# Kernel tuning notes

Hardware: AMD Instinct MI355X
Metric: run time of the kernel (lower is better)

The kernel has to match this reference:

```python
import jax, jax.numpy as jnp
import numpy as np

RANK = 16
ALPHA = 32
SCALING = ALPHA / RANK  # 2.0


def setup_inputs() -> dict:
    key = jax.random.key(0)
    k1, k2, k3 = jax.random.split(key, 3)
    B_, S, D, O = 2, 4096, 4096, 4096
    x = jax.random.normal(k1, (B_, S, D), dtype=jnp.float32)
    # Dequantized base weight, torch Linear layout [out, in]
    W_base = jax.random.normal(k2, (O, D), dtype=jnp.float32) * 0.02
    # kaiming_uniform-ish init for lora_A [rank, in]
    bound = float(np.sqrt(6.0 / (1 + 5) / D))
    A = jax.random.uniform(k3, (RANK, D), dtype=jnp.float32, minval=-bound, maxval=bound)
    # lora_B initialized to zeros [out, rank]
    Bm = jnp.zeros((O, RANK), dtype=jnp.float32)
    return {"x": x, "W_base": W_base, "A": A, "B": Bm}


def reference(x, W_base, A, B):
    # Y = x @ W_base^T + (x @ A^T) @ B^T * scaling   (dropout p=0 -> identity)
    base_out = jnp.einsum('bsd,od->bso', x, W_base)
    lora_mid = jnp.einsum('bsd,rd->bsr', x, A)        # [B,S,rank]
    lora_out = jnp.einsum('bsr,or->bso', lora_mid, B) # [B,S,out]
    return base_out + lora_out * SCALING
```

## Files before the change

### kernel.cpp

```cpp
#include <hip/hip_runtime.h>
#include <hip/hip_bf16.h>

typedef __attribute__((ext_vector_type(8))) __bf16 bf16x8;
typedef __attribute__((ext_vector_type(4))) float  f32x4;

__global__ __launch_bounds__(256) void cvt_f32_bf16(
    const float* __restrict__ in, __bf16* __restrict__ out, long n8)
{
    long i = (long)blockIdx.x * blockDim.x + threadIdx.x;
    long stride = (long)gridDim.x * blockDim.x;
    for (; i < n8; i += stride) {
        const f32x4* p = (const f32x4*)(in + i * 8);
        f32x4 a = p[0], b = p[1];
        bf16x8 o;
        o[0] = (__bf16)a[0]; o[1] = (__bf16)a[1];
        o[2] = (__bf16)a[2]; o[3] = (__bf16)a[3];
        o[4] = (__bf16)b[0]; o[5] = (__bf16)b[1];
        o[6] = (__bf16)b[2]; o[7] = (__bf16)b[3];
        *(bf16x8*)(out + i * 8) = o;
    }
}

__global__ __launch_bounds__(256) void mid_and_cvt(
    const float* __restrict__ x, const float* __restrict__ A,
    float* __restrict__ mid, __bf16* __restrict__ Xb, int K, int M)
{
    int tid = threadIdx.x;
    int m0 = blockIdx.x * 4;

    float acc[4][16];
#pragma unroll
    for (int row = 0; row < 4; ++row)
#pragma unroll
        for (int r = 0; r < 16; ++r) acc[row][r] = 0.f;

    int iters = K / 2048;
    for (int it = 0; it < iters; ++it) {
        int k = it * 2048 + tid * 8;
        f32x4 xv[4][2];
#pragma unroll
        for (int row = 0; row < 4; ++row) {
            if (m0 + row < M) {
                const float* xr = x + (size_t)(m0 + row) * K;
                xv[row][0] = *(const f32x4*)(xr + k);
                xv[row][1] = *(const f32x4*)(xr + k + 4);
            } else {
                f32x4 z = {0.f,0.f,0.f,0.f};
                xv[row][0] = z; xv[row][1] = z;
            }
            if (Xb && m0 + row < M) {
                bf16x8 o;
                o[0] = (__bf16)xv[row][0][0]; o[1] = (__bf16)xv[row][0][1];
                o[2] = (__bf16)xv[row][0][2]; o[3] = (__bf16)xv[row][0][3];
                o[4] = (__bf16)xv[row][1][0]; o[5] = (__bf16)xv[row][1][1];
                o[6] = (__bf16)xv[row][1][2]; o[7] = (__bf16)xv[row][1][3];
                *(bf16x8*)(Xb + (size_t)(m0 + row) * K + k) = o;
            }
        }
#pragma unroll
        for (int r = 0; r < 16; ++r) {
            const f32x4* ap = (const f32x4*)(A + (size_t)r * K + k);
            f32x4 a0 = ap[0], a1 = ap[1];
#pragma unroll
            for (int row = 0; row < 4; ++row) {
                acc[row][r] += xv[row][0][0]*a0[0] + xv[row][0][1]*a0[1]
                             + xv[row][0][2]*a0[2] + xv[row][0][3]*a0[3]
                             + xv[row][1][0]*a1[0] + xv[row][1][1]*a1[1]
                             + xv[row][1][2]*a1[2] + xv[row][1][3]*a1[3];
            }
        }
    }

#pragma unroll
    for (int row = 0; row < 4; ++row)
#pragma unroll
        for (int r = 0; r < 16; ++r)
#pragma unroll
            for (int off = 32; off > 0; off >>= 1)
                acc[row][r] += __shfl_down(acc[row][r], off, 64);

    __shared__ float red[4][4][16];
    int lane = tid & 63, w = tid >> 6;
    if (lane == 0) {
#pragma unroll
        for (int row = 0; row < 4; ++row)
#pragma unroll
            for (int r = 0; r < 16; ++r) red[w][row][r] = acc[row][r];
    }
    __syncthreads();
    if (tid < 64) {
        int row = tid >> 4, r = tid & 15;
        if (m0 + row < M) {
            float s = red[0][row][r] + red[1][row][r]
                    + red[2][row][r] + red[3][row][r];
            mid[(size_t)(m0 + row) * 16 + r] = s;
        }
    }
}

#define GL16(g, l) __builtin_amdgcn_global_load_lds( \
    (const __attribute__((address_space(1))) void*)(g), \
    (__attribute__((address_space(3))) void*)(l), 16, 0, 0)

__global__ __launch_bounds__(512, 2) void gemm256(
    const __bf16* __restrict__ Xb,
    const __bf16* __restrict__ Wb,
    const float*  __restrict__ mid,
    const float*  __restrict__ Bl,
    float* __restrict__ out,
    int M, int N, int K)
{
    __shared__ __bf16 As[4][256 * 32];
    __shared__ __bf16 Bs[4][256 * 32];

    const int NT = K >> 5;

    int nbx = N >> 8, nby = M >> 8, nwg = nbx * nby;
    int bid = blockIdx.x, swz = bid;
    if ((nwg & 7) == 0) { int cpx = nwg >> 3; swz = (bid & 7) * cpx + (bid >> 3); }
    int by = swz / nbx, bx = swz % nbx;
    int m0 = by << 8, n0 = bx << 8;

    int tid = threadIdx.x;
    int lane = tid & 63;
    int w = tid >> 6;
    int wm = w >> 2, wn = w & 3;

    int q0 = tid >> 2;
    int c0 = tid & 3;
    int csrc = c0 ^ ((q0 >> 1) & 3);
    const __bf16* sA0 = Xb + (size_t)(m0 + q0) * K + csrc * 8;
    const __bf16* sA1 = sA0 + (size_t)128 * K;
    const __bf16* sB0 = Wb + (size_t)(n0 + q0) * K + csrc * 8;
    const __bf16* sB1 = sB0 + (size_t)128 * K;
    unsigned ldsw = (unsigned)w * 1024;

    int chunkSwz = (lane >> 4) ^ ((lane >> 1) & 3);
    unsigned aoff = (unsigned)((wm * 128 + (lane & 15)) * 64 + chunkSwz * 16);
    unsigned boff = (unsigned)((wn * 64  + (lane & 15)) * 64 + chunkSwz * 16);

    f32x4 acc[8][4];
    {
        int kh = lane >> 4;
        bf16x8 bI[4];
#pragma unroll
        for (int j = 0; j < 4; ++j) {
            bf16x8 v = {};
            if (kh < 2) {
                int col = n0 + wn * 64 + j * 16 + (lane & 15);
                const f32x4* p = (const f32x4*)(Bl + (size_t)col * 16 + kh * 8);
                f32x4 v0 = p[0], v1 = p[1];
                v[0] = (__bf16)(2.0f * v0[0]); v[1] = (__bf16)(2.0f * v0[1]);
                v[2] = (__bf16)(2.0f * v0[2]); v[3] = (__bf16)(2.0f * v0[3]);
                v[4] = (__bf16)(2.0f * v1[0]); v[5] = (__bf16)(2.0f * v1[1]);
                v[6] = (__bf16)(2.0f * v1[2]); v[7] = (__bf16)(2.0f * v1[3]);
            }
            bI[j] = v;
        }
#pragma unroll
        for (int i = 0; i < 8; ++i) {
            bf16x8 aI = {};
            if (kh < 2) {
                int row = m0 + wm * 128 + i * 16 + (lane & 15);
                const f32x4* p = (const f32x4*)(mid + (size_t)row * 16 + kh * 8);
                f32x4 v0 = p[0], v1 = p[1];
                aI[0] = (__bf16)v0[0]; aI[1] = (__bf16)v0[1];
                aI[2] = (__bf16)v0[2]; aI[3] = (__bf16)v0[3];
                aI[4] = (__bf16)v1[0]; aI[5] = (__bf16)v1[1];
                aI[6] = (__bf16)v1[2]; aI[7] = (__bf16)v1[3];
            }
            f32x4 z = {0.f, 0.f, 0.f, 0.f};
#pragma unroll
            for (int j = 0; j < 4; ++j)
                acc[i][j] = __builtin_amdgcn_mfma_f32_16x16x32_bf16(aI, bI[j], z, 0, 0, 0);
        }
    }

    GL16(sA0, (char*)As[0] + ldsw);
    GL16(sA1, (char*)As[0] + 8192 + ldsw);
    GL16(sB0, (char*)Bs[0] + ldsw);
    GL16(sB1, (char*)Bs[0] + 8192 + ldsw);
    GL16(sA0 + 32, (char*)As[1] + ldsw);
    GL16(sA1 + 32, (char*)As[1] + 8192 + ldsw);
    GL16(sB0 + 32, (char*)Bs[1] + ldsw);
    GL16(sB1 + 32, (char*)Bs[1] + 8192 + ldsw);
    asm volatile("s_waitcnt vmcnt(4)" ::: "memory");
    asm volatile("s_barrier" ::: "memory");

    int cur = 0;
    for (int t = 0; t < NT; ++t) {
        const __bf16* bufA = As[cur];
        const __bf16* bufB = Bs[cur];
        bool pf = (t + 2) < NT;
        int pb = (t + 2) & 3;
        size_t koff = (size_t)(t + 2) * 32;

        if (pf) {
            GL16(sA0 + koff, (char*)As[pb] + ldsw);
            GL16(sA1 + koff, (char*)As[pb] + 8192 + ldsw);
            GL16(sB0 + koff, (char*)Bs[pb] + ldsw);
            GL16(sB1 + koff, (char*)Bs[pb] + 8192 + ldsw);
        }

        bf16x8 bfr[4], af[8];
#pragma unroll
        for (int j = 0; j < 4; ++j)
            bfr[j] = *(const bf16x8*)((const char*)bufB + boff + j * 1024u);
#pragma unroll
        for (int i = 0; i < 8; ++i)
            af[i] = *(const bf16x8*)((const char*)bufA + aoff + i * 1024u);

        __builtin_amdgcn_s_setprio(1);
#pragma unroll
        for (int i = 0; i < 8; ++i)
#pragma unroll
            for (int j = 0; j < 4; ++j)
                acc[i][j] = __builtin_amdgcn_mfma_f32_16x16x32_bf16(
                    af[i], bfr[j], acc[i][j], 0, 0, 0);
        __builtin_amdgcn_s_setprio(0);

        if (pf) asm volatile("s_waitcnt vmcnt(4)" ::: "memory");
        else    asm volatile("s_waitcnt vmcnt(0)" ::: "memory");
        asm volatile("s_barrier" ::: "memory");

        cur = (cur + 1) & 3;
    }

#pragma unroll
    for (int i = 0; i < 8; ++i) {
        int rbase = m0 + wm * 128 + i * 16 + ((lane >> 4) << 2);
#pragma unroll
        for (int q = 0; q < 4; ++q) {
            float* orow = out + (size_t)(rbase + q) * N;
            int colb = n0 + wn * 64 + (lane & 15);
            orow[colb]      = acc[i][0][q];
            orow[colb + 16] = acc[i][1][q];
            orow[colb + 32] = acc[i][2][q];
            orow[colb + 48] = acc[i][3][q];
        }
    }
}

__global__ __launch_bounds__(256) void gemm_fb(
    const float* __restrict__ X, const float* __restrict__ W,
    const float* __restrict__ mid, const float* __restrict__ Bl,
    float* __restrict__ out, int M, int N, int K)
{
    __shared__ float As[64][16];
    __shared__ float Bs[64][16];
    int nbx = N / 64;
    int bx = blockIdx.x % nbx, by = blockIdx.x / nbx;
    int m0 = by * 64, n0 = bx * 64;
    int tid = threadIdx.x;
    int tr = tid >> 4, tc = tid & 15;

    float acc[4][4] = {};
    for (int kt = 0; kt < K; kt += 16) {
#pragma unroll
        for (int s = 0; s < 4; ++s) {
            int c = s * 256 + tid;
            int row = c >> 4, kk = c & 15;
            As[row][kk] = X[(size_t)(m0 + row) * K + kt + kk];
            Bs[row][kk] = W[(size_t)(n0 + row) * K + kt + kk];
        }
        __syncthreads();
#pragma unroll
        for (int kk = 0; kk < 16; ++kk) {
            float av[4], bv[4];
#pragma unroll
            for (int i = 0; i < 4; ++i) { av[i] = As[tr*4+i][kk]; bv[i] = Bs[tc*4+i][kk]; }
#pragma unroll
            for (int i = 0; i < 4; ++i)
#pragma unroll
                for (int j = 0; j < 4; ++j) acc[i][j] += av[i] * bv[j];
        }
        __syncthreads();
    }
#pragma unroll
    for (int i = 0; i < 4; ++i) {
        int row = m0 + tr * 4 + i;
#pragma unroll
        for (int j = 0; j < 4; ++j) {
            int col = n0 + tc * 4 + j;
            float s = 0.f;
#pragma unroll
            for (int r = 0; r < 16; ++r)
                s += mid[(size_t)row * 16 + r] * Bl[(size_t)col * 16 + r];
            out[(size_t)row * N + col] = acc[i][j] + 2.0f * s;
        }
    }
}

extern "C" void kernel_launch(void* const* d_in, const int* in_sizes, int n_in,
                              void* d_out, int out_size, void* d_ws, size_t ws_size,
                              hipStream_t stream)
{
    const float* x   = (const float*)d_in[0];
    const float* Wf  = (const float*)d_in[1];
    const float* A   = (const float*)d_in[2];
    const float* Bl  = (const float*)d_in[3];
    float* out = (float*)d_out;

    int D = in_sizes[2] / 16;
    int O = in_sizes[3] / 16;
    long M = (long)in_sizes[0] / D;
    int K = D, N = O;

    size_t xb_bytes  = (size_t)M * K * 2;
    size_t wb_bytes  = (size_t)N * K * 2;
    size_t mid_bytes = (size_t)M * 16 * 4;

    bool shapes_ok = (M % 256 == 0) && (N % 256 == 0) && (K % 2048 == 0);

    int midgrid = (int)((M + 3) / 4);

    if (shapes_ok && ws_size >= xb_bytes + wb_bytes + mid_bytes) {
        __bf16* Xb  = (__bf16*)d_ws;
        __bf16* Wbb = (__bf16*)((char*)d_ws + xb_bytes);
        float*  mid = (float*)((char*)d_ws + xb_bytes + wb_bytes);

        cvt_f32_bf16<<<2048, 256, 0, stream>>>(Wf, Wbb, (long)N * K / 8);
        mid_and_cvt<<<midgrid, 256, 0, stream>>>(x, A, mid, Xb, K, (int)M);
        int nwg = (int)(M / 256) * (N / 256);
        gemm256<<<nwg, 512, 0, stream>>>(Xb, Wbb, mid, Bl, out, (int)M, N, K);
    } else {
        float* mid = (float*)d_ws;
        mid_and_cvt<<<midgrid, 256, 0, stream>>>(x, A, mid, nullptr, K, (int)M);
        int nwg = (int)(M / 64) * (N / 64);
        gemm_fb<<<nwg, 256, 0, stream>>>(x, Wf, mid, Bl, out, (int)M, N, K);
    }
}
```

Measured before the change: 405.9 us.

## Software-pipeline LDS fragment loads with MFMA in half-tile phases, unroll by two

Restructures the main K loop of the 256x256 GEMM into an unrolled-by-two, four-phase schedule. LDS fragment reads for the next half-tile and the split A/B global_load_lds prefetches are interleaved between groups of 16 MFMAs. The goal is to hide LDS read latency behind matrix work, in the style of ping-pong scheduling. The cost is more barriers per iteration, higher register pressure from double fragment sets, and a dependence on NT being even plus careful vmcnt accounting.

```diff
diff --git a/kernel.cpp b/kernel.cpp
--- a/kernel.cpp
+++ b/kernel.cpp
@@ -102,6 +102,8 @@
     (const __attribute__((address_space(1))) void*)(g), \
     (__attribute__((address_space(3))) void*)(l), 16, 0, 0)
 
+#define LD8(base, off) (*(const bf16x8*)((const char*)(base) + (off)))
+
 __global__ __launch_bounds__(512, 2) void gemm256(
     const __bf16* __restrict__ Xb,
     const __bf16* __restrict__ Wb,
@@ -138,6 +140,13 @@
     int chunkSwz = (lane >> 4) ^ ((lane >> 1) & 3);
     unsigned aoff = (unsigned)((wm * 128 + (lane & 15)) * 64 + chunkSwz * 16);
     unsigned boff = (unsigned)((wn * 64  + (lane & 15)) * 64 + chunkSwz * 16);
+
+#define STAGE_A(t, b) do { size_t ko = (size_t)(t) * 32; \
+    GL16(sA0 + ko, (char*)As[b] + ldsw); \
+    GL16(sA1 + ko, (char*)As[b] + 8192 + ldsw); } while (0)
+#define STAGE_B(t, b) do { size_t ko = (size_t)(t) * 32; \
+    GL16(sB0 + ko, (char*)Bs[b] + ldsw); \
+    GL16(sB1 + ko, (char*)Bs[b] + 8192 + ldsw); } while (0)
 
     f32x4 acc[8][4];
     {
@@ -176,54 +185,142 @@
         }
     }
 
-    GL16(sA0, (char*)As[0] + ldsw);
-    GL16(sA1, (char*)As[0] + 8192 + ldsw);
-    GL16(sB0, (char*)Bs[0] + ldsw);
-    GL16(sB1, (char*)Bs[0] + 8192 + ldsw);
-    GL16(sA0 + 32, (char*)As[1] + ldsw);
-    GL16(sA1 + 32, (char*)As[1] + 8192 + ldsw);
-    GL16(sB0 + 32, (char*)Bs[1] + ldsw);
-    GL16(sB1 + 32, (char*)Bs[1] + 8192 + ldsw);
+    STAGE_A(0, 0); STAGE_B(0, 0);
+    STAGE_A(1, 1); STAGE_B(1, 1);
     asm volatile("s_waitcnt vmcnt(4)" ::: "memory");
     asm volatile("s_barrier" ::: "memory");
 
-    int cur = 0;
-    for (int t = 0; t < NT; ++t) {
-        const __bf16* bufA = As[cur];
-        const __bf16* bufB = Bs[cur];
-        bool pf = (t + 2) < NT;
-        int pb = (t + 2) & 3;
-        size_t koff = (size_t)(t + 2) * 32;
-
-        if (pf) {
-            GL16(sA0 + koff, (char*)As[pb] + ldsw);
-            GL16(sA1 + koff, (char*)As[pb] + 8192 + ldsw);
-            GL16(sB0 + koff, (char*)Bs[pb] + ldsw);
-            GL16(sB1 + koff, (char*)Bs[pb] + 8192 + ldsw);
-        }
-
-        bf16x8 bfr[4], af[8];
-#pragma unroll
-        for (int j = 0; j < 4; ++j)
-            bfr[j] = *(const bf16x8*)((const char*)bufB + boff + j * 1024u);
-#pragma unroll
-        for (int i = 0; i < 8; ++i)
-            af[i] = *(const bf16x8*)((const char*)bufA + aoff + i * 1024u);
-
+    bf16x8 axf0 = LD8(As[0], aoff);
+    bf16x8 axf1 = LD8(As[0], aoff + 1024);
+    bf16x8 axf2 = LD8(As[0], aoff + 2048);
+    bf16x8 axf3 = LD8(As[0], aoff + 3072);
+    bf16x8 bxf0 = LD8(Bs[0], boff);
+    bf16x8 bxf1 = LD8(Bs[0], boff + 1024);
+    bf16x8 bxf2 = LD8(Bs[0], boff + 2048);
+    bf16x8 bxf3 = LD8(Bs[0], boff + 3072);
+
+    for (int t = 0; t < NT; t += 2) {
+        const char* cA0 = (const char*)As[t & 3];
+        const char* cA1 = (const char*)As[(t + 1) & 3];
+        const char* cB1 = (const char*)Bs[(t + 1) & 3];
+        const char* cA2 = (const char*)As[(t + 2) & 3];
+        const char* cB2 = (const char*)Bs[(t + 2) & 3];
+        bool p2 = (t + 2) < NT;
+        bool p3 = (t + 3) < NT;
+
+        bf16x8 ax4 = LD8(cA0, aoff + 4096);
+        bf16x8 ax5 = LD8(cA0, aoff + 5120);
+        bf16x8 ax6 = LD8(cA0, aoff + 6144);
+        bf16x8 ax7 = LD8(cA0, aoff + 7168);
+        if (p2) STAGE_A(t + 2, (t + 2) & 3);
+        asm volatile("s_barrier" ::: "memory");
         __builtin_amdgcn_s_setprio(1);
-#pragma unroll
-        for (int i = 0; i < 8; ++i)
-#pragma unroll
-            for (int j = 0; j < 4; ++j)
-                acc[i][j] = __builtin_amdgcn_mfma_f32_16x16x32_bf16(
-                    af[i], bfr[j], acc[i][j], 0, 0, 0);
+        acc[0][0] = __builtin_amdgcn_mfma_f32_16x16x32_bf16(axf0, bxf0, acc[0][0], 0, 0, 0);
+        acc[0][1] = __builtin_amdgcn_mfma_f32_16x16x32_bf16(axf0, bxf1, acc[0][1], 0, 0, 0);
+        acc[0][2] = __builtin_amdgcn_mfma_f32_16x16x32_bf16(axf0, bxf2, acc[0][2], 0, 0, 0);
+        acc[0][3] = __builtin_amdgcn_mfma_f32_16x16x32_bf16(axf0, bxf3, acc[0][3], 0, 0, 0);
+        acc[1][0] = __builtin_amdgcn_mfma_f32_16x16x32_bf16(axf1, bxf0, acc[1][0], 0, 0, 0);
+        acc[1][1] = __builtin_amdgcn_mfma_f32_16x16x32_bf16(axf1, bxf1, acc[1][1], 0, 0, 0);
+        acc[1][2] = __builtin_amdgcn_mfma_f32_16x16x32_bf16(axf1, bxf2, acc[1][2], 0, 0, 0);
+        acc[1][3] = __builtin_amdgcn_mfma_f32_16x16x32_bf16(axf1, bxf3, acc[1][3], 0, 0, 0);
+        acc[2][0] = __builtin_amdgcn_mfma_f32_16x16x32_bf16(axf2, bxf0, acc[2][0], 0, 0, 0);
+        acc[2][1] = __builtin_amdgcn_mfma_f32_16x16x32_bf16(axf2, bxf1, acc[2][1], 0, 0, 0);
+        acc[2][2] = __builtin_amdgcn_mfma_f32_16x16x32_bf16(axf2, bxf2, acc[2][2], 0, 0, 0);
+        acc[2][3] = __builtin_amdgcn_mfma_f32_16x16x32_bf16(axf2, bxf3, acc[2][3], 0, 0, 0);
+        acc[3][0] = __builtin_amdgcn_mfma_f32_16x16x32_bf16(axf3, bxf0, acc[3][0], 0, 0, 0);
+        acc[3][1] = __builtin_amdgcn_mfma_f32_16x16x32_bf16(axf3, bxf1, acc[3][1], 0, 0, 0);
+        acc[3][2] = __builtin_amdgcn_mfma_f32_16x16x32_bf16(axf3, bxf2, acc[3][2], 0, 0, 0);
+        acc[3][3] = __builtin_amdgcn_mfma_f32_16x16x32_bf16(axf3, bxf3, acc[3][3], 0, 0, 0);
         __builtin_amdgcn_s_setprio(0);
 
-        if (pf) asm volatile("s_waitcnt vmcnt(4)" ::: "memory");
+        if (p2) STAGE_B(t + 2, (t + 2) & 3);
+        if (p2) asm volatile("s_waitcnt vmcnt(4)" ::: "memory");
         else    asm volatile("s_waitcnt vmcnt(0)" ::: "memory");
+        bf16x8 ayf0 = LD8(cA1, aoff);
+        bf16x8 ayf1 = LD8(cA1, aoff + 1024);
+        bf16x8 ayf2 = LD8(cA1, aoff + 2048);
+        bf16x8 ayf3 = LD8(cA1, aoff + 3072);
+        bf16x8 byf0 = LD8(cB1, boff);
+        bf16x8 byf1 = LD8(cB1, boff + 1024);
+        bf16x8 byf2 = LD8(cB1, boff + 2048);
+        bf16x8 byf3 = LD8(cB1, boff + 3072);
         asm volatile("s_barrier" ::: "memory");
-
-        cur = (cur + 1) & 3;
+        __builtin_amdgcn_s_setprio(1);
+        acc[4][0] = __builtin_amdgcn_mfma_f32_16x16x32_bf16(ax4, bxf0, acc[4][0], 0, 0, 0);
+        acc[4][1] = __builtin_amdgcn_mfma_f32_16x16x32_bf16(ax4, bxf1, acc[4][1], 0, 0, 0);
+        acc[4][2] = __builtin_amdgcn_mfma_f32_16x16x32_bf16(ax4, bxf2, acc[4][2], 0, 0, 0);
+        acc[4][3] = __builtin_amdgcn_mfma_f32_16x16x32_bf16(ax4, bxf3, acc[4][3], 0, 0, 0);
+        acc[5][0] = __builtin_amdgcn_mfma_f32_16x16x32_bf16(ax5, bxf0, acc[5][0], 0, 0, 0);
+        acc[5][1] = __builtin_amdgcn_mfma_f32_16x16x32_bf16(ax5, bxf1, acc[5][1], 0, 0, 0);
+        acc[5][2] = __builtin_amdgcn_mfma_f32_16x16x32_bf16(ax5, bxf2, acc[5][2], 0, 0, 0);
+        acc[5][3] = __builtin_amdgcn_mfma_f32_16x16x32_bf16(ax5, bxf3, acc[5][3], 0, 0, 0);
+        acc[6][0] = __builtin_amdgcn_mfma_f32_16x16x32_bf16(ax6, bxf0, acc[6][0], 0, 0, 0);
+        acc[6][1] = __builtin_amdgcn_mfma_f32_16x16x32_bf16(ax6, bxf1, acc[6][1], 0, 0, 0);
+        acc[6][2] = __builtin_amdgcn_mfma_f32_16x16x32_bf16(ax6, bxf2, acc[6][2], 0, 0, 0);
+        acc[6][3] = __builtin_amdgcn_mfma_f32_16x16x32_bf16(ax6, bxf3, acc[6][3], 0, 0, 0);
+        acc[7][0] = __builtin_amdgcn_mfma_f32_16x16x32_bf16(ax7, bxf0, acc[7][0], 0, 0, 0);
+        acc[7][1] = __builtin_amdgcn_mfma_f32_16x16x32_bf16(ax7, bxf1, acc[7][1], 0, 0, 0);
+        acc[7][2] = __builtin_amdgcn_mfma_f32_16x16x32_bf16(ax7, bxf2, acc[7][2], 0, 0, 0);
+        acc[7][3] = __builtin_amdgcn_mfma_f32_16x16x32_bf16(ax7, bxf3, acc[7][3], 0, 0, 0);
+        __builtin_amdgcn_s_setprio(0);
+
+        bf16x8 ay4 = LD8(cA1, aoff + 4096);
+        bf16x8 ay5 = LD8(cA1, aoff + 5120);
+        bf16x8 ay6 = LD8(cA1, aoff + 6144);
+        bf16x8 ay7 = LD8(cA1, aoff + 7168);
+        if (p3) STAGE_A(t + 3, (t + 3) & 3);
+        asm volatile("s_barrier" ::: "memory");
+        __builtin_amdgcn_s_setprio(1);
+        acc[0][0] = __builtin_amdgcn_mfma_f32_16x16x32_bf16(ayf0, byf0, acc[0][0], 0, 0, 0);
+        acc[0][1] = __builtin_amdgcn_mfma_f32_16x16x32_bf16(ayf0, byf1, acc[0][1], 0, 0, 0);
+        acc[0][2] = __builtin_amdgcn_mfma_f32_16x16x32_bf16(ayf0, byf2, acc[0][2], 0, 0, 0);
+        acc[0][3] = __builtin_amdgcn_mfma_f32_16x16x32_bf16(ayf0, byf3, acc[0][3], 0, 0, 0);
+        acc[1][0] = __builtin_amdgcn_mfma_f32_16x16x32_bf16(ayf1, byf0, acc[1][0], 0, 0, 0);
+        acc[1][1] = __builtin_amdgcn_mfma_f32_16x16x32_bf16(ayf1, byf1, acc[1][1], 0, 0, 0);
+        acc[1][2] = __builtin_amdgcn_mfma_f32_16x16x32_bf16(ayf1, byf2, acc[1][2], 0, 0, 0);
+        acc[1][3] = __builtin_amdgcn_mfma_f32_16x16x32_bf16(ayf1, byf3, acc[1][3], 0, 0, 0);
+        acc[2][0] = __builtin_amdgcn_mfma_f32_16x16x32_bf16(ayf2, byf0, acc[2][0], 0, 0, 0);
+        acc[2][1] = __builtin_amdgcn_mfma_f32_16x16x32_bf16(ayf2, byf1, acc[2][1], 0, 0, 0);
+        acc[2][2] = __builtin_amdgcn_mfma_f32_16x16x32_bf16(ayf2, byf2, acc[2][2], 0, 0, 0);
+        acc[2][3] = __builtin_amdgcn_mfma_f32_16x16x32_bf16(ayf2, byf3, acc[2][3], 0, 0, 0);
+        acc[3][0] = __builtin_amdgcn_mfma_f32_16x16x32_bf16(ayf3, byf0, acc[3][0], 0, 0, 0);
+        acc[3][1] = __builtin_amdgcn_mfma_f32_16x16x32_bf16(ayf3, byf1, acc[3][1], 0, 0, 0);
+        acc[3][2] = __builtin_amdgcn_mfma_f32_16x16x32_bf16(ayf3, byf2, acc[3][2], 0, 0, 0);
+        acc[3][3] = __builtin_amdgcn_mfma_f32_16x16x32_bf16(ayf3, byf3, acc[3][3], 0, 0, 0);
+        __builtin_amdgcn_s_setprio(0);
+
+        if (p3) STAGE_B(t + 3, (t + 3) & 3);
+        if (p3) asm volatile("s_waitcnt vmcnt(4)" ::: "memory");
+        else    asm volatile("s_waitcnt vmcnt(0)" ::: "memory");
+        if (p2) {
+            axf0 = LD8(cA2, aoff);
+            axf1 = LD8(cA2, aoff + 1024);
+            axf2 = LD8(cA2, aoff + 2048);
+            axf3 = LD8(cA2, aoff + 3072);
+            bxf0 = LD8(cB2, boff);
+            bxf1 = LD8(cB2, boff + 1024);
+            bxf2 = LD8(cB2, boff + 2048);
+            bxf3 = LD8(cB2, boff + 3072);
+        }
+        asm volatile("s_barrier" ::: "memory");
+        __builtin_amdgcn_s_setprio(1);
+        acc[4][0] = __builtin_amdgcn_mfma_f32_16x16x32_bf16(ay4, byf0, acc[4][0], 0, 0, 0);
+        acc[4][1] = __builtin_amdgcn_mfma_f32_16x16x32_bf16(ay4, byf1, acc[4][1], 0, 0, 0);
+        acc[4][2] = __builtin_amdgcn_mfma_f32_16x16x32_bf16(ay4, byf2, acc[4][2], 0, 0, 0);
+        acc[4][3] = __builtin_amdgcn_mfma_f32_16x16x32_bf16(ay4, byf3, acc[4][3], 0, 0, 0);
+        acc[5][0] = __builtin_amdgcn_mfma_f32_16x16x32_bf16(ay5, byf0, acc[5][0], 0, 0, 0);
+        acc[5][1] = __builtin_amdgcn_mfma_f32_16x16x32_bf16(ay5, byf1, acc[5][1], 0, 0, 0);
+        acc[5][2] = __builtin_amdgcn_mfma_f32_16x16x32_bf16(ay5, byf2, acc[5][2], 0, 0, 0);
+        acc[5][3] = __builtin_amdgcn_mfma_f32_16x16x32_bf16(ay5, byf3, acc[5][3], 0, 0, 0);
+        acc[6][0] = __builtin_amdgcn_mfma_f32_16x16x32_bf16(ay6, byf0, acc[6][0], 0, 0, 0);
+        acc[6][1] = __builtin_amdgcn_mfma_f32_16x16x32_bf16(ay6, byf1, acc[6][1], 0, 0, 0);
+        acc[6][2] = __builtin_amdgcn_mfma_f32_16x16x32_bf16(ay6, byf2, acc[6][2], 0, 0, 0);
+        acc[6][3] = __builtin_amdgcn_mfma_f32_16x16x32_bf16(ay6, byf3, acc[6][3], 0, 0, 0);
+        acc[7][0] = __builtin_amdgcn_mfma_f32_16x16x32_bf16(ay7, byf0, acc[7][0], 0, 0, 0);
+        acc[7][1] = __builtin_amdgcn_mfma_f32_16x16x32_bf16(ay7, byf1, acc[7][1], 0, 0, 0);
+        acc[7][2] = __builtin_amdgcn_mfma_f32_16x16x32_bf16(ay7, byf2, acc[7][2], 0, 0, 0);
+        acc[7][3] = __builtin_amdgcn_mfma_f32_16x16x32_bf16(ay7, byf3, acc[7][3], 0, 0, 0);
+        __builtin_amdgcn_s_setprio(0);
     }
 
 #pragma unroll
```

Result: faster. 344.2 us (-15.2%).
